# Kernel tuning notes

Hardware: AMD Instinct MI355X
Metric: run time of the kernel (lower is better)

## Reference

```python
import jax, jax.numpy as jnp
import numpy as np

B, N, DIN, DOUT, H = 4, 2048, 256, 256, 4
HD = DOUT // H
NEG_SLOPE = 0.2


def setup_inputs() -> dict:
    key = jax.random.key(0)
    k1, k2, k3, k4, k5 = jax.random.split(key, 5)
    x = jax.random.normal(k1, (B, N, DIN), dtype=jnp.float32)
    adj = jax.random.randint(k2, (B, N, N), 0, 2).astype(jnp.float32)
    # ensure self-loops so every softmax row has at least one valid entry
    adj = jnp.maximum(adj, jnp.eye(N, dtype=jnp.float32)[None])
    # xavier-uniform-ish scales
    w_bound = float(np.sqrt(6.0 / (DIN + DOUT)))
    a_bound = float(np.sqrt(6.0 / (1 + HD)))
    W = jax.random.uniform(k3, (DOUT, DIN), jnp.float32, -w_bound, w_bound)
    a_src = jax.random.uniform(k4, (H, HD), jnp.float32, -a_bound, a_bound)
    a_dst = jax.random.uniform(k5, (H, HD), jnp.float32, -a_bound, a_bound)
    return {"x": x, "adj": adj, "W": W, "a_src": a_src, "a_dst": a_dst}


def reference(x, adj, W, a_src, a_dst):
    b, n, _ = x.shape
    h = (x @ W.T).reshape(b, n, H, HD)                      # [B,N,H,HD]
    s_src = jnp.einsum('bnhd,hd->bnh', h, a_src)            # [B,N,H]
    s_dst = jnp.einsum('bnhd,hd->bnh', h, a_dst)            # [B,N,H]
    # e[b,i,j,h] = leaky_relu(s_src[b,i,h] + s_dst[b,j,h])
    e = jax.nn.leaky_relu(s_src[:, :, None, :] + s_dst[:, None, :, :], NEG_SLOPE)
    e = jnp.where(adj[..., None] == 0, -jnp.inf, e)         # [B,N,N,H]
    alpha = jax.nn.softmax(e, axis=2)                       # softmax over j (dropout is identity at eval)
    out = jnp.einsum('bijh,bjhd->bihd', alpha, h)           # weighted aggregate
    return out.reshape(b, n, DOUT)
```

## Files before the change

### kernel.cpp

```cpp
#include <hip/hip_runtime.h>
#include <math.h>

#define Bb   4
#define Nn   2048
#define Dd   256
#define Hh   4
#define HDd  64
#define BN   (Bb * Nn)

typedef float v4f __attribute__((ext_vector_type(4)));
typedef short v8s __attribute__((ext_vector_type(8)));

__device__ __forceinline__ unsigned rne_bf16(float f) {
    unsigned u = __float_as_uint(f);
    u += 0x7fffu + ((u >> 16) & 1u);
    return u >> 16;
}

__global__ __launch_bounds__(256, 2) void k_gemm(const float* __restrict__ x,
                                                 const float* __restrict__ W,
                                                 const float* __restrict__ a_src,
                                                 const float* __restrict__ a_dst,
                                                 const float* __restrict__ adj,
                                                 unsigned short* __restrict__ hbf,
                                                 float* __restrict__ ssrc,
                                                 float* __restrict__ sdst,
                                                 unsigned long long* __restrict__ bitadj) {
    __shared__ __align__(16) unsigned short xs[2][64 * 72];
    __shared__ __align__(16) unsigned short wsm[2][64 * 72];
    __shared__ float asd[128];

    const int bid0 = (int)blockIdx.x;
    if (bid0 & 1) {
        const int gw = (bid0 >> 1) * 4 + ((int)threadIdx.x >> 6);
        const int lane = (int)threadIdx.x & 63;
#pragma unroll 1
        for (int w = gw * 4; w < 262144; w += 2048 * 4) {
            float v0 = adj[(size_t)((w + 0) >> 5) * 2048 + ((w + 0) & 31) * 64 + lane];
            float v1 = adj[(size_t)((w + 1) >> 5) * 2048 + ((w + 1) & 31) * 64 + lane];
            float v2 = adj[(size_t)((w + 2) >> 5) * 2048 + ((w + 2) & 31) * 64 + lane];
            float v3 = adj[(size_t)((w + 3) >> 5) * 2048 + ((w + 3) & 31) * 64 + lane];
            unsigned long long m0 = __ballot(v0 != 0.0f);
            unsigned long long m1 = __ballot(v1 != 0.0f);
            unsigned long long m2 = __ballot(v2 != 0.0f);
            unsigned long long m3 = __ballot(v3 != 0.0f);
            if (lane == 0) {
                bitadj[w + 0] = m0;
                bitadj[w + 1] = m1;
                bitadj[w + 2] = m2;
                bitadj[w + 3] = m3;
            }
        }
        return;
    }

    const int g = bid0 >> 1;
    const int head = (g >> 2) & 3;
    const int mtile = (g & 3) + 4 * (g >> 4);
    const int tid = threadIdx.x;
    const int m0 = mtile * 64;
    const int n0 = head * 64;
    const int b = m0 >> 11;
    const int i0loc = m0 & 2047;

    if (tid < 128) {
        int sel = tid >> 6, d = tid & 63;
        asd[tid] = sel ? a_dst[n0 + d] : a_src[n0 + d];
    }

    const int wv = tid >> 6, ln = tid & 63, l15 = ln & 15, l4 = ln >> 4;
    const int mh = wv >> 1, nh = wv & 1;
    const int srow = tid >> 2, kq = (tid & 3) * 16;

    v4f acc[2][2];
#pragma unroll
    for (int gg = 0; gg < 2; ++gg)
#pragma unroll
        for (int t = 0; t < 2; ++t) acc[gg][t] = (v4f){0.f, 0.f, 0.f, 0.f};

    for (int st = 0; st < 4; ++st) {
        const int k0 = st * 64;
        __syncthreads();
        {
            float xf[16], wf[16];
            const float* xp = x + (size_t)(m0 + srow) * Dd + k0 + kq;
            const float* wp = W + (size_t)(n0 + srow) * Dd + k0 + kq;
#pragma unroll
            for (int q = 0; q < 4; ++q) {
                *(float4*)&xf[q * 4] = *(const float4*)(xp + q * 4);
                *(float4*)&wf[q * 4] = *(const float4*)(wp + q * 4);
            }
            unsigned xh[8], xl[8], wh[8], wl[8];
#pragma unroll
            for (int j = 0; j < 8; ++j) {
                unsigned h0 = rne_bf16(xf[2 * j]), h1 = rne_bf16(xf[2 * j + 1]);
                float l0 = xf[2 * j] - __uint_as_float(h0 << 16);
                float l1 = xf[2 * j + 1] - __uint_as_float(h1 << 16);
                xh[j] = h0 | (h1 << 16);
                xl[j] = rne_bf16(l0) | (rne_bf16(l1) << 16);
                unsigned g0 = rne_bf16(wf[2 * j]), g1 = rne_bf16(wf[2 * j + 1]);
                float m0f = wf[2 * j] - __uint_as_float(g0 << 16);
                float m1f = wf[2 * j + 1] - __uint_as_float(g1 << 16);
                wh[j] = g0 | (g1 << 16);
                wl[j] = rne_bf16(m0f) | (rne_bf16(m1f) << 16);
            }
            *(uint4*)(xs[0] + srow * 72 + kq)     = make_uint4(xh[0], xh[1], xh[2], xh[3]);
            *(uint4*)(xs[0] + srow * 72 + kq + 8) = make_uint4(xh[4], xh[5], xh[6], xh[7]);
            *(uint4*)(xs[1] + srow * 72 + kq)     = make_uint4(xl[0], xl[1], xl[2], xl[3]);
            *(uint4*)(xs[1] + srow * 72 + kq + 8) = make_uint4(xl[4], xl[5], xl[6], xl[7]);
            *(uint4*)(wsm[0] + srow * 72 + kq)     = make_uint4(wh[0], wh[1], wh[2], wh[3]);
            *(uint4*)(wsm[0] + srow * 72 + kq + 8) = make_uint4(wh[4], wh[5], wh[6], wh[7]);
            *(uint4*)(wsm[1] + srow * 72 + kq)     = make_uint4(wl[0], wl[1], wl[2], wl[3]);
            *(uint4*)(wsm[1] + srow * 72 + kq + 8) = make_uint4(wl[4], wl[5], wl[6], wl[7]);
        }
        __syncthreads();
        {
            v8s ah[2][2], al[2][2], bh_[2][2], bl_[2][2];
#pragma unroll
            for (int gg = 0; gg < 2; ++gg)
#pragma unroll
                for (int kh = 0; kh < 2; ++kh) {
                    int ro = (mh * 32 + gg * 16 + l15) * 72 + kh * 32 + l4 * 8;
                    ah[gg][kh] = *(const v8s*)(xs[0] + ro);
                    al[gg][kh] = *(const v8s*)(xs[1] + ro);
                }
#pragma unroll
            for (int t = 0; t < 2; ++t)
#pragma unroll
                for (int kh = 0; kh < 2; ++kh) {
                    int ro = (nh * 32 + t * 16 + l15) * 72 + kh * 32 + l4 * 8;
                    bh_[t][kh] = *(const v8s*)(wsm[0] + ro);
                    bl_[t][kh] = *(const v8s*)(wsm[1] + ro);
                }
#pragma unroll
            for (int gg = 0; gg < 2; ++gg)
#pragma unroll
                for (int t = 0; t < 2; ++t)
#pragma unroll
                    for (int kh = 0; kh < 2; ++kh) {
                        acc[gg][t] = __builtin_amdgcn_mfma_f32_16x16x32_bf16(ah[gg][kh], bh_[t][kh], acc[gg][t], 0, 0, 0);
                        acc[gg][t] = __builtin_amdgcn_mfma_f32_16x16x32_bf16(al[gg][kh], bh_[t][kh], acc[gg][t], 0, 0, 0);
                        acc[gg][t] = __builtin_amdgcn_mfma_f32_16x16x32_bf16(ah[gg][kh], bl_[t][kh], acc[gg][t], 0, 0, 0);
                    }
        }
    }

    __syncthreads();
    float* T = (float*)&xs[0][0];
#pragma unroll
    for (int gg = 0; gg < 2; ++gg)
#pragma unroll
        for (int t = 0; t < 2; ++t)
#pragma unroll
            for (int r = 0; r < 4; ++r) {
                int d = nh * 32 + t * 16 + l15;
                int m = mh * 32 + gg * 16 + l4 * 4 + r;
                T[d * 67 + m] = acc[gg][t][r];
            }
    __syncthreads();
    if (tid < 128) {
        int m = tid & 63, sel = tid >> 6;
        float s = 0.f;
#pragma unroll
        for (int d = 0; d < 64; ++d) s += T[d * 67 + m] * asd[sel * 64 + d];
        (sel ? sdst : ssrc)[(size_t)head * BN + (size_t)b * Nn + i0loc + m] = s;
        int dloc = tid >> 1, jh2 = tid & 1;
        const float* row = T + dloc * 67 + jh2 * 32;
        unsigned pk[16];
#pragma unroll
        for (int jj = 0; jj < 16; ++jj)
            pk[jj] = rne_bf16(row[jj * 2]) | (rne_bf16(row[jj * 2 + 1]) << 16);
        const int jb = (i0loc >> 5) + jh2;
        const int dt = dloc >> 4, fl = dloc & 15;
        unsigned short* rb = hbf +
            ((size_t)((b * 64 + jb) * 4 + head) * 2048 + dt * 512 + fl * 8);
        *(uint4*)(rb + 0 * 128) = make_uint4(pk[0],  pk[1],  pk[2],  pk[3]);
        *(uint4*)(rb + 1 * 128) = make_uint4(pk[4],  pk[5],  pk[6],  pk[7]);
        *(uint4*)(rb + 2 * 128) = make_uint4(pk[8],  pk[9],  pk[10], pk[11]);
        *(uint4*)(rb + 3 * 128) = make_uint4(pk[12], pk[13], pk[14], pk[15]);
    }
}

__global__ __launch_bounds__(512, 4) void k_aggr(const unsigned short* __restrict__ hbf,
                                                 const unsigned long long* __restrict__ bitadj,
                                                 const float* __restrict__ ssrc,
                                                 const float* __restrict__ sdst,
                                                 float* __restrict__ out) {
    __shared__ __align__(16) unsigned short Btile[2][4][2048];
    __shared__ __align__(16) float dtab[2048 * 2];
    __shared__ __align__(16) float red[4][64][20];

    const int tid = threadIdx.x;
    const int bid = (int)blockIdx.x;
    const int xcd  = bid & 7;
    const int h    = xcd >> 1;
    const int bpar = xcd & 1;
    const int q    = bid >> 3;
    const int b    = ((q & 1) << 1) | bpar;
    const int itile = q >> 1;
    const int i0 = itile * 64;

    const int wv   = tid >> 6;
    const int isub = wv >> 1;
    const int jp   = wv & 1;
    const int ln = tid & 63, l15 = ln & 15, l4 = ln >> 4;

    const int ri   = (tid >> 7) & 3;
    const int soff = (tid & 127) * 16;

    {
        const int j4 = tid * 4;
        float4 sv = *(const float4*)(sdst + (size_t)h * BN + (size_t)b * Nn + j4);
        float4 o0 = make_float4(__expf(sv.x), __expf(0.2f * sv.x),
                                __expf(sv.y), __expf(0.2f * sv.y));
        float4 o1 = make_float4(__expf(sv.z), __expf(0.2f * sv.z),
                                __expf(sv.w), __expf(0.2f * sv.w));
        *(float4*)&dtab[j4 * 2]     = o0;
        *(float4*)&dtab[j4 * 2 + 4] = o1;
    }

    const int irow = i0 + isub * 16 + l15;
    const float ss = ssrc[(size_t)h * BN + (size_t)b * Nn + irow];
    const float c1 = __expf(ss), c2 = __expf(0.2f * ss);
    const unsigned char* ajr = (const unsigned char*)bitadj +
        ((size_t)b * Nn + irow) * 256;
    const unsigned short* sb2 = hbf +
        ((size_t)(b * 64 * 4) + h) * 2048 + soff;
    const float* dtb = dtab + l4 * 16;

    const v8s ones = {0x3F80, 0x3F80, 0x3F80, 0x3F80, 0x3F80, 0x3F80, 0x3F80, 0x3F80};

    v4f acc0 = (v4f){0.f, 0.f, 0.f, 0.f}, acc1 = acc0, acc2 = acc0, acc3 = acc0, zac = acc0;
    uint4 stg0, stg1;
    unsigned mA, mB;

#define GENFRAG(dst, M_, dd_) do {                                            \
        const float4 q0_ = *(const float4*)((dd_) + 0);                       \
        const float4 q1_ = *(const float4*)((dd_) + 4);                       \
        const float4 q2_ = *(const float4*)((dd_) + 8);                       \
        const float4 q3_ = *(const float4*)((dd_) + 12);                      \
        float w0_ = ((M_) & 1u)   ? fmaxf(c1 * q0_.x, c2 * q0_.y) : 0.f;      \
        float w1_ = ((M_) & 2u)   ? fmaxf(c1 * q0_.z, c2 * q0_.w) : 0.f;      \
        float w2_ = ((M_) & 4u)   ? fmaxf(c1 * q1_.x, c2 * q1_.y) : 0.f;      \
        float w3_ = ((M_) & 8u)   ? fmaxf(c1 * q1_.z, c2 * q1_.w) : 0.f;      \
        float w4_ = ((M_) & 16u)  ? fmaxf(c1 * q2_.x, c2 * q2_.y) : 0.f;      \
        float w5_ = ((M_) & 32u)  ? fmaxf(c1 * q2_.z, c2 * q2_.w) : 0.f;      \
        float w6_ = ((M_) & 64u)  ? fmaxf(c1 * q3_.x, c2 * q3_.y) : 0.f;      \
        float w7_ = ((M_) & 128u) ? fmaxf(c1 * q3_.z, c2 * q3_.w) : 0.f;      \
        union { v8s v; unsigned u[4]; } P_;                                   \
        asm("v_cvt_pk_bf16_f32 %0, %1, %2" : "=v"(P_.u[0]) : "v"(w0_), "v"(w1_)); \
        asm("v_cvt_pk_bf16_f32 %0, %1, %2" : "=v"(P_.u[1]) : "v"(w2_), "v"(w3_)); \
        asm("v_cvt_pk_bf16_f32 %0, %1, %2" : "=v"(P_.u[2]) : "v"(w4_), "v"(w5_)); \
        asm("v_cvt_pk_bf16_f32 %0, %1, %2" : "=v"(P_.u[3]) : "v"(w6_), "v"(w7_)); \
        dst = P_.v;                                                           \
    } while (0)

#define COMPUTE(JC_, M_, btp) do {                                            \
        const unsigned short* bp_ = (btp);                                    \
        v8s bf0_ = *(const v8s*)(bp_ + 0 * 512 + ln * 8);                     \
        v8s bf1_ = *(const v8s*)(bp_ + 1 * 512 + ln * 8);                     \
        v8s bf2_ = *(const v8s*)(bp_ + 2 * 512 + ln * 8);                     \
        v8s bf3_ = *(const v8s*)(bp_ + 3 * 512 + ln * 8);                     \
        const float* dd_ = dtb + (JC_) * 64;                                  \
        v8s afr_;                                                             \
        GENFRAG(afr_, M_, dd_);                                               \
        acc0 = __builtin_amdgcn_mfma_f32_16x16x32_bf16(afr_, bf0_, acc0, 0, 0, 0); \
        acc1 = __builtin_amdgcn_mfma_f32_16x16x32_bf16(afr_, bf1_, acc1, 0, 0, 0); \
        acc2 = __builtin_amdgcn_mfma_f32_16x16x32_bf16(afr_, bf2_, acc2, 0, 0, 0); \
        acc3 = __builtin_amdgcn_mfma_f32_16x16x32_bf16(afr_, bf3_, acc3, 0, 0, 0); \
        zac  = __builtin_amdgcn_mfma_f32_16x16x32_bf16(afr_, ones, zac,  0, 0, 0); \
    } while (0)

    stg0 = *(const uint4*)(sb2 + (size_t)ri * 8192);
    stg1 = *(const uint4*)(sb2 + (size_t)ri * 8192 + 8);
    mA = ajr[jp * 4 + l4];
    mB = ajr[(2 + jp) * 4 + l4];
    *(uint4*)&Btile[0][ri][soff]     = stg0;
    *(uint4*)&Btile[0][ri][soff + 8] = stg1;
    __syncthreads();

#pragma unroll 1
    for (int sr = 0; sr < 16; ++sr) {
        const int buf = sr & 1;
        const int jq = ((sr + 1) & 15) * 4;
        stg0 = *(const uint4*)(sb2 + (size_t)(jq + ri) * 8192);
        stg1 = *(const uint4*)(sb2 + (size_t)(jq + ri) * 8192 + 8);
        const unsigned mA2 = ajr[(jq + jp) * 4 + l4];
        const unsigned mB2 = ajr[(jq + 2 + jp) * 4 + l4];
        __builtin_amdgcn_sched_barrier(0);
        COMPUTE(4 * sr + jp,     mA, Btile[buf][jp]);
        COMPUTE(4 * sr + 2 + jp, mB, Btile[buf][2 + jp]);
        *(uint4*)&Btile[buf ^ 1][ri][soff]     = stg0;
        *(uint4*)&Btile[buf ^ 1][ri][soff + 8] = stg1;
        mA = mA2; mB = mB2;
        __syncthreads();
    }

#undef GENFRAG
#undef COMPUTE

    if (jp) {
        float* rp = &red[isub][ln][0];
        *(v4f*)(rp + 0)  = acc0;
        *(v4f*)(rp + 4)  = acc1;
        *(v4f*)(rp + 8)  = acc2;
        *(v4f*)(rp + 12) = acc3;
        *(v4f*)(rp + 16) = zac;
    }
    __syncthreads();
    if (!jp) {
        const float* rp = &red[isub][ln][0];
        acc0 += *(const v4f*)(rp + 0);
        acc1 += *(const v4f*)(rp + 4);
        acc2 += *(const v4f*)(rp + 8);
        acc3 += *(const v4f*)(rp + 12);
        zac  += *(const v4f*)(rp + 16);
        float* op = out + ((size_t)b * Nn + i0 + isub * 16 + l4 * 4) * Dd + h * HDd + l15;
#pragma unroll
        for (int r = 0; r < 4; ++r) {
            float zi = 1.f / zac[r];
            op[(size_t)r * Dd + 0]  = acc0[r] * zi;
            op[(size_t)r * Dd + 16] = acc1[r] * zi;
            op[(size_t)r * Dd + 32] = acc2[r] * zi;
            op[(size_t)r * Dd + 48] = acc3[r] * zi;
        }
    }
}

extern "C" void kernel_launch(void* const* d_in, const int* in_sizes, int n_in,
                              void* d_out, int out_size, void* d_ws, size_t ws_size,
                              hipStream_t stream) {
    const float* x     = (const float*)d_in[0];
    const float* adj   = (const float*)d_in[1];
    const float* W     = (const float*)d_in[2];
    const float* a_src = (const float*)d_in[3];
    const float* a_dst = (const float*)d_in[4];
    float* out = (float*)d_out;

    unsigned short* hbf = (unsigned short*)d_ws;
    float* ssrc = (float*)(hbf + (size_t)Bb * Nn * Dd);
    float* sdst = ssrc + (size_t)Hh * BN;
    unsigned long long* bitadj = (unsigned long long*)(sdst + (size_t)Hh * BN);

    k_gemm<<<dim3(1024), dim3(256), 0, stream>>>(x, W, a_src, a_dst, adj,
                                                 hbf, ssrc, sdst, bitadj);
    k_aggr<<<dim3(512), dim3(512), 0, stream>>>(hbf, bitadj, ssrc, sdst, out);
}
```

Measured before the change: 137.9 us.

## Fuse projection, adjacency packing and aggregation into one kernel with flag sync

Merges the GEMM/bit-packing kernel and the aggregation kernel into a single 512-block launch. The first 256 blocks compute the projection, with each block covering two M tiles that share one W tile; the rest pack the adjacency matrix into bitmasks. Each block signals completion through per-(batch, head) and per-batch atomic counters, and all blocks then spin-wait on those counters before running their aggregation tile. This removes the gap between the two launches and lets later batches' work overlap with earlier aggregation. In exchange it adds a memset launch and relies on every block being co-resident, since the spin-waits would deadlock otherwise.

```diff
diff --git a/kernel.cpp b/kernel.cpp
--- a/kernel.cpp
+++ b/kernel.cpp
@@ -17,25 +17,185 @@
     return u >> 16;
 }
 
-__global__ __launch_bounds__(256, 2) void k_gemm(const float* __restrict__ x,
-                                                 const float* __restrict__ W,
-                                                 const float* __restrict__ a_src,
-                                                 const float* __restrict__ a_dst,
-                                                 const float* __restrict__ adj,
-                                                 unsigned short* __restrict__ hbf,
-                                                 float* __restrict__ ssrc,
-                                                 float* __restrict__ sdst,
-                                                 unsigned long long* __restrict__ bitadj) {
-    __shared__ __align__(16) unsigned short xs[2][64 * 72];
-    __shared__ __align__(16) unsigned short wsm[2][64 * 72];
-    __shared__ float asd[128];
-
-    const int bid0 = (int)blockIdx.x;
-    if (bid0 & 1) {
-        const int gw = (bid0 >> 1) * 4 + ((int)threadIdx.x >> 6);
-        const int lane = (int)threadIdx.x & 63;
+__global__ __launch_bounds__(512, 4) void k_fused(const float* __restrict__ x,
+                                                  const float* __restrict__ W,
+                                                  const float* __restrict__ a_src,
+                                                  const float* __restrict__ a_dst,
+                                                  const float* __restrict__ adj,
+                                                  unsigned short* __restrict__ hbf,
+                                                  float* __restrict__ ssrc,
+                                                  float* __restrict__ sdst,
+                                                  unsigned long long* __restrict__ bitadj,
+                                                  unsigned* __restrict__ flags,
+                                                  float* __restrict__ out) {
+    __shared__ __align__(16) union {
+        struct {
+            unsigned short xs[2][2][4608];
+            unsigned short wsm[2][4608];
+            float asd[128];
+        } p1;
+        struct {
+            unsigned short Btile[2][4][2048];
+            float dtab[4096];
+            float red[4][64][20];
+        } p2;
+    } sm;
+
+    const int tid = threadIdx.x;
+    const int bid = (int)blockIdx.x;
+
+    if (bid < 256) {
+        const int head = bid & 3;
+        const int mt2  = bid >> 2;
+        const int half = tid >> 8;
+        const int tl   = tid & 255;
+        const int mtile = mt2 * 2 + half;
+        const int m0 = mtile * 64;
+        const int n0 = head * 64;
+        const int b = m0 >> 11;
+        const int i0loc = m0 & 2047;
+
+        if (tid < 128) {
+            int sel = tid >> 6, d = tid & 63;
+            sm.p1.asd[tid] = sel ? a_dst[n0 + d] : a_src[n0 + d];
+        }
+
+        unsigned short* xsh = sm.p1.xs[half][0];
+        unsigned short* xsl = sm.p1.xs[half][1];
+        unsigned short* wh0 = sm.p1.wsm[0];
+        unsigned short* wl0 = sm.p1.wsm[1];
+
+        const int wv = tl >> 6, ln = tl & 63, l15 = ln & 15, l4 = ln >> 4;
+        const int mh = wv >> 1, nh = wv & 1;
+        const int srow = tl >> 2, kq = (tl & 3) * 16;
+
+        v4f acc[2][2];
+#pragma unroll
+        for (int gg = 0; gg < 2; ++gg)
+#pragma unroll
+            for (int t = 0; t < 2; ++t) acc[gg][t] = (v4f){0.f, 0.f, 0.f, 0.f};
+
+        for (int st = 0; st < 4; ++st) {
+            const int k0 = st * 64;
+            __syncthreads();
+            {
+                float xf[16];
+                const float* xp = x + (size_t)(m0 + srow) * Dd + k0 + kq;
+#pragma unroll
+                for (int q = 0; q < 4; ++q)
+                    *(float4*)&xf[q * 4] = *(const float4*)(xp + q * 4);
+                unsigned xh[8], xl8[8];
+#pragma unroll
+                for (int j = 0; j < 8; ++j) {
+                    unsigned h0 = rne_bf16(xf[2 * j]), h1 = rne_bf16(xf[2 * j + 1]);
+                    float l0 = xf[2 * j] - __uint_as_float(h0 << 16);
+                    float l1 = xf[2 * j + 1] - __uint_as_float(h1 << 16);
+                    xh[j] = h0 | (h1 << 16);
+                    xl8[j] = rne_bf16(l0) | (rne_bf16(l1) << 16);
+                }
+                *(uint4*)(xsh + srow * 72 + kq)     = make_uint4(xh[0], xh[1], xh[2], xh[3]);
+                *(uint4*)(xsh + srow * 72 + kq + 8) = make_uint4(xh[4], xh[5], xh[6], xh[7]);
+                *(uint4*)(xsl + srow * 72 + kq)     = make_uint4(xl8[0], xl8[1], xl8[2], xl8[3]);
+                *(uint4*)(xsl + srow * 72 + kq + 8) = make_uint4(xl8[4], xl8[5], xl8[6], xl8[7]);
+                if (half == 0) {
+                    float wf[16];
+                    const float* wp = W + (size_t)(n0 + srow) * Dd + k0 + kq;
+#pragma unroll
+                    for (int q = 0; q < 4; ++q)
+                        *(float4*)&wf[q * 4] = *(const float4*)(wp + q * 4);
+                    unsigned wh[8], wl[8];
+#pragma unroll
+                    for (int j = 0; j < 8; ++j) {
+                        unsigned g0 = rne_bf16(wf[2 * j]), g1 = rne_bf16(wf[2 * j + 1]);
+                        float m0f = wf[2 * j] - __uint_as_float(g0 << 16);
+                        float m1f = wf[2 * j + 1] - __uint_as_float(g1 << 16);
+                        wh[j] = g0 | (g1 << 16);
+                        wl[j] = rne_bf16(m0f) | (rne_bf16(m1f) << 16);
+                    }
+                    *(uint4*)(wh0 + srow * 72 + kq)     = make_uint4(wh[0], wh[1], wh[2], wh[3]);
+                    *(uint4*)(wh0 + srow * 72 + kq + 8) = make_uint4(wh[4], wh[5], wh[6], wh[7]);
+                    *(uint4*)(wl0 + srow * 72 + kq)     = make_uint4(wl[0], wl[1], wl[2], wl[3]);
+                    *(uint4*)(wl0 + srow * 72 + kq + 8) = make_uint4(wl[4], wl[5], wl[6], wl[7]);
+                }
+            }
+            __syncthreads();
+            {
+                v8s ah[2][2], al[2][2], bh_[2][2], bl_[2][2];
+#pragma unroll
+                for (int gg = 0; gg < 2; ++gg)
+#pragma unroll
+                    for (int kh = 0; kh < 2; ++kh) {
+                        int ro = (mh * 32 + gg * 16 + l15) * 72 + kh * 32 + l4 * 8;
+                        ah[gg][kh] = *(const v8s*)(xsh + ro);
+                        al[gg][kh] = *(const v8s*)(xsl + ro);
+                    }
+#pragma unroll
+                for (int t = 0; t < 2; ++t)
+#pragma unroll
+                    for (int kh = 0; kh < 2; ++kh) {
+                        int ro = (nh * 32 + t * 16 + l15) * 72 + kh * 32 + l4 * 8;
+                        bh_[t][kh] = *(const v8s*)(wh0 + ro);
+                        bl_[t][kh] = *(const v8s*)(wl0 + ro);
+                    }
+#pragma unroll
+                for (int gg = 0; gg < 2; ++gg)
+#pragma unroll
+                    for (int t = 0; t < 2; ++t)
+#pragma unroll
+                        for (int kh = 0; kh < 2; ++kh) {
+                            acc[gg][t] = __builtin_amdgcn_mfma_f32_16x16x32_bf16(ah[gg][kh], bh_[t][kh], acc[gg][t], 0, 0, 0);
+                            acc[gg][t] = __builtin_amdgcn_mfma_f32_16x16x32_bf16(al[gg][kh], bh_[t][kh], acc[gg][t], 0, 0, 0);
+                            acc[gg][t] = __builtin_amdgcn_mfma_f32_16x16x32_bf16(ah[gg][kh], bl_[t][kh], acc[gg][t], 0, 0, 0);
+                        }
+            }
+        }
+
+        __syncthreads();
+        float* T = (float*)xsh;
+#pragma unroll
+        for (int gg = 0; gg < 2; ++gg)
+#pragma unroll
+            for (int t = 0; t < 2; ++t)
+#pragma unroll
+                for (int r = 0; r < 4; ++r) {
+                    int d = nh * 32 + t * 16 + l15;
+                    int m = mh * 32 + gg * 16 + l4 * 4 + r;
+                    T[d * 67 + m] = acc[gg][t][r];
+                }
+        __syncthreads();
+        if (tl < 128) {
+            int m = tl & 63, sel = tl >> 6;
+            float s = 0.f;
+#pragma unroll
+            for (int d = 0; d < 64; ++d) s += T[d * 67 + m] * sm.p1.asd[sel * 64 + d];
+            (sel ? sdst : ssrc)[(size_t)head * BN + (size_t)b * Nn + i0loc + m] = s;
+            int dloc = tl >> 1, jh2 = tl & 1;
+            const float* row = T + dloc * 67 + jh2 * 32;
+            unsigned pk[16];
+#pragma unroll
+            for (int jj = 0; jj < 16; ++jj)
+                pk[jj] = rne_bf16(row[jj * 2]) | (rne_bf16(row[jj * 2 + 1]) << 16);
+            const int jb = (i0loc >> 5) + jh2;
+            const int dt = dloc >> 4, fl = dloc & 15;
+            unsigned short* rb = hbf +
+                ((size_t)((b * 64 + jb) * 4 + head) * 2048 + dt * 512 + fl * 8);
+            *(uint4*)(rb + 0 * 128) = make_uint4(pk[0],  pk[1],  pk[2],  pk[3]);
+            *(uint4*)(rb + 1 * 128) = make_uint4(pk[4],  pk[5],  pk[6],  pk[7]);
+            *(uint4*)(rb + 2 * 128) = make_uint4(pk[8],  pk[9],  pk[10], pk[11]);
+            *(uint4*)(rb + 3 * 128) = make_uint4(pk[12], pk[13], pk[14], pk[15]);
+        }
+        __syncthreads();
+        if (tid == 0) {
+            __threadfence();
+            atomicAdd(&flags[b * 4 + head], 1u);
+        }
+    } else {
+        const int c  = bid - 256;
+        const int cb = c >> 6;
+        const int w0 = cb * 65536 + (c & 63) * 1024 + (tid >> 6) * 128;
+        const int lane = tid & 63;
 #pragma unroll 1
-        for (int w = gw * 4; w < 262144; w += 2048 * 4) {
+        for (int w = w0; w < w0 + 128; w += 4) {
             float v0 = adj[(size_t)((w + 0) >> 5) * 2048 + ((w + 0) & 31) * 64 + lane];
             float v1 = adj[(size_t)((w + 1) >> 5) * 2048 + ((w + 1) & 31) * 64 + lane];
             float v2 = adj[(size_t)((w + 2) >> 5) * 2048 + ((w + 2) & 31) * 64 + lane];
@@ -51,154 +211,28 @@
                 bitadj[w + 3] = m3;
             }
         }
-        return;
-    }
-
-    const int g = bid0 >> 1;
-    const int head = (g >> 2) & 3;
-    const int mtile = (g & 3) + 4 * (g >> 4);
-    const int tid = threadIdx.x;
-    const int m0 = mtile * 64;
-    const int n0 = head * 64;
-    const int b = m0 >> 11;
-    const int i0loc = m0 & 2047;
-
-    if (tid < 128) {
-        int sel = tid >> 6, d = tid & 63;
-        asd[tid] = sel ? a_dst[n0 + d] : a_src[n0 + d];
-    }
-
-    const int wv = tid >> 6, ln = tid & 63, l15 = ln & 15, l4 = ln >> 4;
-    const int mh = wv >> 1, nh = wv & 1;
-    const int srow = tid >> 2, kq = (tid & 3) * 16;
-
-    v4f acc[2][2];
-#pragma unroll
-    for (int gg = 0; gg < 2; ++gg)
-#pragma unroll
-        for (int t = 0; t < 2; ++t) acc[gg][t] = (v4f){0.f, 0.f, 0.f, 0.f};
-
-    for (int st = 0; st < 4; ++st) {
-        const int k0 = st * 64;
-        __syncthreads();
-        {
-            float xf[16], wf[16];
-            const float* xp = x + (size_t)(m0 + srow) * Dd + k0 + kq;
-            const float* wp = W + (size_t)(n0 + srow) * Dd + k0 + kq;
-#pragma unroll
-            for (int q = 0; q < 4; ++q) {
-                *(float4*)&xf[q * 4] = *(const float4*)(xp + q * 4);
-                *(float4*)&wf[q * 4] = *(const float4*)(wp + q * 4);
-            }
-            unsigned xh[8], xl[8], wh[8], wl[8];
-#pragma unroll
-            for (int j = 0; j < 8; ++j) {
-                unsigned h0 = rne_bf16(xf[2 * j]), h1 = rne_bf16(xf[2 * j + 1]);
-                float l0 = xf[2 * j] - __uint_as_float(h0 << 16);
-                float l1 = xf[2 * j + 1] - __uint_as_float(h1 << 16);
-                xh[j] = h0 | (h1 << 16);
-                xl[j] = rne_bf16(l0) | (rne_bf16(l1) << 16);
-                unsigned g0 = rne_bf16(wf[2 * j]), g1 = rne_bf16(wf[2 * j + 1]);
-                float m0f = wf[2 * j] - __uint_as_float(g0 << 16);
-                float m1f = wf[2 * j + 1] - __uint_as_float(g1 << 16);
-                wh[j] = g0 | (g1 << 16);
-                wl[j] = rne_bf16(m0f) | (rne_bf16(m1f) << 16);
-            }
-            *(uint4*)(xs[0] + srow * 72 + kq)     = make_uint4(xh[0], xh[1], xh[2], xh[3]);
-            *(uint4*)(xs[0] + srow * 72 + kq + 8) = make_uint4(xh[4], xh[5], xh[6], xh[7]);
-            *(uint4*)(xs[1] + srow * 72 + kq)     = make_uint4(xl[0], xl[1], xl[2], xl[3]);
-            *(uint4*)(xs[1] + srow * 72 + kq + 8) = make_uint4(xl[4], xl[5], xl[6], xl[7]);
-            *(uint4*)(wsm[0] + srow * 72 + kq)     = make_uint4(wh[0], wh[1], wh[2], wh[3]);
-            *(uint4*)(wsm[0] + srow * 72 + kq + 8) = make_uint4(wh[4], wh[5], wh[6], wh[7]);
-            *(uint4*)(wsm[1] + srow * 72 + kq)     = make_uint4(wl[0], wl[1], wl[2], wl[3]);
-            *(uint4*)(wsm[1] + srow * 72 + kq + 8) = make_uint4(wl[4], wl[5], wl[6], wl[7]);
-        }
-        __syncthreads();
-        {
-            v8s ah[2][2], al[2][2], bh_[2][2], bl_[2][2];
-#pragma unroll
-            for (int gg = 0; gg < 2; ++gg)
-#pragma unroll
-                for (int kh = 0; kh < 2; ++kh) {
-                    int ro = (mh * 32 + gg * 16 + l15) * 72 + kh * 32 + l4 * 8;
-                    ah[gg][kh] = *(const v8s*)(xs[0] + ro);
-                    al[gg][kh] = *(const v8s*)(xs[1] + ro);
-                }
-#pragma unroll
-            for (int t = 0; t < 2; ++t)
-#pragma unroll
-                for (int kh = 0; kh < 2; ++kh) {
-                    int ro = (nh * 32 + t * 16 + l15) * 72 + kh * 32 + l4 * 8;
-                    bh_[t][kh] = *(const v8s*)(wsm[0] + ro);
-                    bl_[t][kh] = *(const v8s*)(wsm[1] + ro);
-                }
-#pragma unroll
-            for (int gg = 0; gg < 2; ++gg)
-#pragma unroll
-                for (int t = 0; t < 2; ++t)
-#pragma unroll
-                    for (int kh = 0; kh < 2; ++kh) {
-                        acc[gg][t] = __builtin_amdgcn_mfma_f32_16x16x32_bf16(ah[gg][kh], bh_[t][kh], acc[gg][t], 0, 0, 0);
-                        acc[gg][t] = __builtin_amdgcn_mfma_f32_16x16x32_bf16(al[gg][kh], bh_[t][kh], acc[gg][t], 0, 0, 0);
-                        acc[gg][t] = __builtin_amdgcn_mfma_f32_16x16x32_bf16(ah[gg][kh], bl_[t][kh], acc[gg][t], 0, 0, 0);
-                    }
-        }
-    }
-
-    __syncthreads();
-    float* T = (float*)&xs[0][0];
-#pragma unroll
-    for (int gg = 0; gg < 2; ++gg)
-#pragma unroll
-        for (int t = 0; t < 2; ++t)
-#pragma unroll
-            for (int r = 0; r < 4; ++r) {
-                int d = nh * 32 + t * 16 + l15;
-                int m = mh * 32 + gg * 16 + l4 * 4 + r;
-                T[d * 67 + m] = acc[gg][t][r];
-            }
-    __syncthreads();
-    if (tid < 128) {
-        int m = tid & 63, sel = tid >> 6;
-        float s = 0.f;
-#pragma unroll
-        for (int d = 0; d < 64; ++d) s += T[d * 67 + m] * asd[sel * 64 + d];
-        (sel ? sdst : ssrc)[(size_t)head * BN + (size_t)b * Nn + i0loc + m] = s;
-        int dloc = tid >> 1, jh2 = tid & 1;
-        const float* row = T + dloc * 67 + jh2 * 32;
-        unsigned pk[16];
-#pragma unroll
-        for (int jj = 0; jj < 16; ++jj)
-            pk[jj] = rne_bf16(row[jj * 2]) | (rne_bf16(row[jj * 2 + 1]) << 16);
-        const int jb = (i0loc >> 5) + jh2;
-        const int dt = dloc >> 4, fl = dloc & 15;
-        unsigned short* rb = hbf +
-            ((size_t)((b * 64 + jb) * 4 + head) * 2048 + dt * 512 + fl * 8);
-        *(uint4*)(rb + 0 * 128) = make_uint4(pk[0],  pk[1],  pk[2],  pk[3]);
-        *(uint4*)(rb + 1 * 128) = make_uint4(pk[4],  pk[5],  pk[6],  pk[7]);
-        *(uint4*)(rb + 2 * 128) = make_uint4(pk[8],  pk[9],  pk[10], pk[11]);
-        *(uint4*)(rb + 3 * 128) = make_uint4(pk[12], pk[13], pk[14], pk[15]);
-    }
-}
-
-__global__ __launch_bounds__(512, 4) void k_aggr(const unsigned short* __restrict__ hbf,
-                                                 const unsigned long long* __restrict__ bitadj,
-                                                 const float* __restrict__ ssrc,
-                                                 const float* __restrict__ sdst,
-                                                 float* __restrict__ out) {
-    __shared__ __align__(16) unsigned short Btile[2][4][2048];
-    __shared__ __align__(16) float dtab[2048 * 2];
-    __shared__ __align__(16) float red[4][64][20];
-
-    const int tid = threadIdx.x;
-    const int bid = (int)blockIdx.x;
+        __syncthreads();
+        if (tid == 0) {
+            __threadfence();
+            atomicAdd(&flags[16 + cb], 1u);
+        }
+    }
+
     const int xcd  = bid & 7;
     const int h    = xcd >> 1;
     const int bpar = xcd & 1;
     const int q    = bid >> 3;
-    const int b    = ((q & 1) << 1) | bpar;
+    const int b2   = ((q & 1) << 1) | bpar;
     const int itile = q >> 1;
     const int i0 = itile * 64;
+
+    if (tid == 0) {
+        while (__hip_atomic_load(&flags[b2 * 4 + h], __ATOMIC_RELAXED, __HIP_MEMORY_SCOPE_AGENT) < 16u ||
+               __hip_atomic_load(&flags[16 + b2],    __ATOMIC_RELAXED, __HIP_MEMORY_SCOPE_AGENT) < 64u)
+            __builtin_amdgcn_s_sleep(2);
+    }
+    __syncthreads();
+    __threadfence();
 
     const int wv   = tid >> 6;
     const int isub = wv >> 1;
@@ -210,23 +244,23 @@
 
     {
         const int j4 = tid * 4;
-        float4 sv = *(const float4*)(sdst + (size_t)h * BN + (size_t)b * Nn + j4);
+        float4 sv = *(const float4*)(sdst + (size_t)h * BN + (size_t)b2 * Nn + j4);
         float4 o0 = make_float4(__expf(sv.x), __expf(0.2f * sv.x),
                                 __expf(sv.y), __expf(0.2f * sv.y));
         float4 o1 = make_float4(__expf(sv.z), __expf(0.2f * sv.z),
                                 __expf(sv.w), __expf(0.2f * sv.w));
-        *(float4*)&dtab[j4 * 2]     = o0;
-        *(float4*)&dtab[j4 * 2 + 4] = o1;
+        *(float4*)&sm.p2.dtab[j4 * 2]     = o0;
+        *(float4*)&sm.p2.dtab[j4 * 2 + 4] = o1;
     }
 
     const int irow = i0 + isub * 16 + l15;
-    const float ss = ssrc[(size_t)h * BN + (size_t)b * Nn + irow];
+    const float ss = ssrc[(size_t)h * BN + (size_t)b2 * Nn + irow];
     const float c1 = __expf(ss), c2 = __expf(0.2f * ss);
     const unsigned char* ajr = (const unsigned char*)bitadj +
-        ((size_t)b * Nn + irow) * 256;
+        ((size_t)b2 * Nn + irow) * 256;
     const unsigned short* sb2 = hbf +
-        ((size_t)(b * 64 * 4) + h) * 2048 + soff;
-    const float* dtb = dtab + l4 * 16;
+        ((size_t)(b2 * 64 * 4) + h) * 2048 + soff;
+    const float* dtb = sm.p2.dtab + l4 * 16;
 
     const v8s ones = {0x3F80, 0x3F80, 0x3F80, 0x3F80, 0x3F80, 0x3F80, 0x3F80, 0x3F80};
 
@@ -275,8 +309,8 @@
     stg1 = *(const uint4*)(sb2 + (size_t)ri * 8192 + 8);
     mA = ajr[jp * 4 + l4];
     mB = ajr[(2 + jp) * 4 + l4];
-    *(uint4*)&Btile[0][ri][soff]     = stg0;
-    *(uint4*)&Btile[0][ri][soff + 8] = stg1;
+    *(uint4*)&sm.p2.Btile[0][ri][soff]     = stg0;
+    *(uint4*)&sm.p2.Btile[0][ri][soff + 8] = stg1;
     __syncthreads();
 
 #pragma unroll 1
@@ -288,10 +322,10 @@
         const unsigned mA2 = ajr[(jq + jp) * 4 + l4];
         const unsigned mB2 = ajr[(jq + 2 + jp) * 4 + l4];
         __builtin_amdgcn_sched_barrier(0);
-        COMPUTE(4 * sr + jp,     mA, Btile[buf][jp]);
-        COMPUTE(4 * sr + 2 + jp, mB, Btile[buf][2 + jp]);
-        *(uint4*)&Btile[buf ^ 1][ri][soff]     = stg0;
-        *(uint4*)&Btile[buf ^ 1][ri][soff + 8] = stg1;
+        COMPUTE(4 * sr + jp,     mA, sm.p2.Btile[buf][jp]);
+        COMPUTE(4 * sr + 2 + jp, mB, sm.p2.Btile[buf][2 + jp]);
+        *(uint4*)&sm.p2.Btile[buf ^ 1][ri][soff]     = stg0;
+        *(uint4*)&sm.p2.Btile[buf ^ 1][ri][soff + 8] = stg1;
         mA = mA2; mB = mB2;
         __syncthreads();
     }
@@ -300,7 +334,7 @@
 #undef COMPUTE
 
     if (jp) {
-        float* rp = &red[isub][ln][0];
+        float* rp = &sm.p2.red[isub][ln][0];
         *(v4f*)(rp + 0)  = acc0;
         *(v4f*)(rp + 4)  = acc1;
         *(v4f*)(rp + 8)  = acc2;
@@ -309,13 +343,13 @@
     }
     __syncthreads();
     if (!jp) {
-        const float* rp = &red[isub][ln][0];
+        const float* rp = &sm.p2.red[isub][ln][0];
         acc0 += *(const v4f*)(rp + 0);
         acc1 += *(const v4f*)(rp + 4);
         acc2 += *(const v4f*)(rp + 8);
         acc3 += *(const v4f*)(rp + 12);
         zac  += *(const v4f*)(rp + 16);
-        float* op = out + ((size_t)b * Nn + i0 + isub * 16 + l4 * 4) * Dd + h * HDd + l15;
+        float* op = out + ((size_t)b2 * Nn + i0 + isub * 16 + l4 * 4) * Dd + h * HDd + l15;
 #pragma unroll
         for (int r = 0; r < 4; ++r) {
             float zi = 1.f / zac[r];
@@ -341,8 +375,9 @@
     float* ssrc = (float*)(hbf + (size_t)Bb * Nn * Dd);
     float* sdst = ssrc + (size_t)Hh * BN;
     unsigned long long* bitadj = (unsigned long long*)(sdst + (size_t)Hh * BN);
-
-    k_gemm<<<dim3(1024), dim3(256), 0, stream>>>(x, W, a_src, a_dst, adj,
-                                                 hbf, ssrc, sdst, bitadj);
-    k_aggr<<<dim3(512), dim3(512), 0, stream>>>(hbf, bitadj, ssrc, sdst, out);
+    unsigned* flags = (unsigned*)(bitadj + 262144);
+
+    hipMemsetAsync(flags, 0, 32 * sizeof(unsigned), stream);
+    k_fused<<<dim3(512), dim3(512), 0, stream>>>(x, W, a_src, a_dst, adj,
+                                                 hbf, ssrc, sdst, bitadj, flags, out);
 }
```

Result: slower. 269.1 us (+95.1%).
